# Optimization experiments

Hardware: AMD Instinct MI355X
Metric: run time of the kernel (lower is better)

Reference implementation:

```python
import jax, jax.numpy as jnp
import numpy as np

U = 100000          # unique pillars
N = 2 * U           # voxels (2 per pillar -> unq_cnt==2, mask all True)
NUM_BINS = 32       # z bins
C_IN = 5
C_HID = 32          # out_channels // 2 in conv1d MLP
C_OUT = 64
R = 4               # channel-attention reduction
K = 7               # bin-attention conv kernel


def setup_inputs() -> dict:
    key = jax.random.key(0)
    ks = jax.random.split(key, 12)
    voxel_features = jax.random.normal(ks[0], (N, C_IN), jnp.float32)
    # each pillar p owns voxels 2p, 2p+1 placed in two distinct bins -> no scatter collision
    bins = (jnp.arange(N, dtype=jnp.int32) % NUM_BINS)
    voxel_coords = jnp.zeros((N, 4), jnp.int32).at[:, 1].set(bins)
    unq_coords = jnp.arange(U, dtype=jnp.int32)
    unq_inv = jnp.arange(N, dtype=jnp.int32) // 2
    unq_cnt = jnp.full((U,), 2, jnp.int32)
    s = 0.3
    return {
        'voxel_features': voxel_features,
        'voxel_coords': voxel_coords,
        'unq_coords': unq_coords,
        'unq_inv': unq_inv,
        'unq_cnt': unq_cnt,
        # up_dimension MLP (Linear(5,32) -> relu -> Linear(32,64))
        'W1': jax.random.normal(ks[1], (C_IN, C_HID), jnp.float32) * s,
        'b1': jnp.zeros((C_HID,), jnp.float32),
        'W2': jax.random.normal(ks[2], (C_HID, C_OUT), jnp.float32) * s,
        'b2': jnp.zeros((C_OUT,), jnp.float32),
        # ZBAM channel-attention shared MLP
        'Wc1': jax.random.normal(ks[3], (C_OUT, C_OUT // R), jnp.float32) * s,
        'bc1': jnp.zeros((C_OUT // R,), jnp.float32),
        'Wc2': jax.random.normal(ks[4], (C_OUT // R, C_OUT), jnp.float32) * s,
        'bc2': jnp.zeros((C_OUT,), jnp.float32),
        # ZBAM bin (spatial) attention: conv1d over bins, 2->1 channels, kernel 7
        'Wsp': jax.random.normal(ks[5], (1, 2, K), jnp.float32) * s,
        'bsp': jnp.zeros((1,), jnp.float32),
    }


def _cbam_forward(voxel_features, W1, b1, W2, b2, Wc1, bc1, Wc2, bc2, Wsp, bsp,
                  voxel_coords, unq_coords, unq_inv, unq_cnt):
    n_pillars = unq_coords.shape[0]
    # --- binning: scatter voxels into (pillar, z-bin) slots ---
    src = jnp.zeros((n_pillars, NUM_BINS, voxel_features.shape[1]), voxel_features.dtype)
    src = src.at[unq_inv, voxel_coords[:, 1]].set(voxel_features)
    occupied_mask = unq_cnt >= 2  # all True by construction -> src[mask] == src
    # --- up_dimension MLP: (U, bins, 5) -> (U, bins, 64) ---
    x = jax.nn.relu(src @ W1 + b1) @ W2 + b2
    x = jnp.transpose(x, (0, 2, 1))  # (U, C, bins)
    # --- ZBAM channel attention ---
    avg_p = x.mean(axis=2)
    max_p = x.max(axis=2)
    mlp = lambda v: jax.nn.relu(v @ Wc1 + bc1) @ Wc2 + bc2
    att_c = jax.nn.sigmoid(mlp(avg_p) + mlp(max_p))  # (U, C)
    x = x * att_c[:, :, None]
    # --- ZBAM bin attention (conv over z-bins) ---
    s = jnp.stack([x.mean(axis=1), x.max(axis=1)], axis=1)  # (U, 2, bins)
    att_s = jax.lax.conv_general_dilated(
        s, Wsp, window_strides=(1,), padding=[(K // 2, K // 2)],
        dimension_numbers=('NCH', 'OIH', 'NCH')) + bsp  # (U, 1, bins)
    x = x * jax.nn.sigmoid(att_s)
    # --- max-pool over bins ---
    return x.max(axis=2), occupied_mask


def reference(voxel_features, voxel_coords, unq_coords, unq_inv, unq_cnt,
              W1, b1, W2, b2, Wc1, bc1, Wc2, bc2, Wsp, bsp):
    return _cbam_forward(voxel_features, W1, b1, W2, b2, Wc1, bc1, Wc2, bc2,
                         Wsp, bsp, voxel_coords, unq_coords, unq_inv, unq_cnt)
```

## Files before the change

kernel.cpp:

```cpp
#include <hip/hip_runtime.h>
#include <math.h>


#define CO 64

typedef __attribute__((ext_vector_type(8))) short s16x8;
typedef __attribute__((ext_vector_type(4))) float f32x4;
union ABu { uint4 u4; s16x8 s; };

__device__ __forceinline__ float sgm(float x) {
  return 1.0f / (1.0f + __expf(-x));
}
template <int PAT>
__device__ __forceinline__ float qadd(float s) {
  int t = __builtin_amdgcn_update_dpp(0, __builtin_bit_cast(int, s),
                                      PAT, 0xf, 0xf, true);
  return s + __builtin_bit_cast(float, t);
}
template <int PAT>
__device__ __forceinline__ float qmaxd(float m) {
  int t = __builtin_amdgcn_update_dpp(__builtin_bit_cast(int, m),
                                      __builtin_bit_cast(int, m),
                                      PAT, 0xf, 0xf, false);
  return fmaxf(m, __builtin_bit_cast(float, t));
}
template <int PAT>
__device__ __forceinline__ float qmind(float m) {
  int t = __builtin_amdgcn_update_dpp(__builtin_bit_cast(int, m),
                                      __builtin_bit_cast(int, m),
                                      PAT, 0xf, 0xf, false);
  return fminf(m, __builtin_bit_cast(float, t));
}
__device__ __forceinline__ float qsum4(float s) { return qadd<0x4E>(qadd<0xB1>(s)); }
__device__ __forceinline__ float qmax4(float m) { return qmaxd<0x4E>(qmaxd<0xB1>(m)); }
__device__ __forceinline__ float qmin4(float m) { return qmind<0x4E>(qmind<0xB1>(m)); }
__device__ __forceinline__ void drain_lds() {
  __builtin_amdgcn_wave_barrier();
  __builtin_amdgcn_s_waitcnt(0xC07F);
  __builtin_amdgcn_wave_barrier();
}
__device__ __forceinline__ void drain_vm() {
  __builtin_amdgcn_wave_barrier();
  __builtin_amdgcn_s_waitcnt(0x0F70);
  __builtin_amdgcn_wave_barrier();
}

__device__ __forceinline__ uint rtn16(float f) {
  uint u = __builtin_bit_cast(uint, f);
  return u + 0x7fffu + ((u >> 16) & 1u);
}
__device__ __forceinline__ void mk_frag(const float* e, ABu& hi, ABu& lo) {
  uint h[4], l[4];
#pragma unroll
  for (int p = 0; p < 4; ++p) {
    uint r0 = rtn16(e[2 * p]), r1 = rtn16(e[2 * p + 1]);
    h[p] = (r0 >> 16) | (r1 & 0xffff0000u);
    float d0 = e[2 * p]     - __builtin_bit_cast(float, r0 & 0xffff0000u);
    float d1 = e[2 * p + 1] - __builtin_bit_cast(float, r1 & 0xffff0000u);
    uint s0 = rtn16(d0), s1 = rtn16(d1);
    l[p] = (s0 >> 16) | (s1 & 0xffff0000u);
  }
  hi.u4 = make_uint4(h[0], h[1], h[2], h[3]);
  lo.u4 = make_uint4(l[0], l[1], l[2], l[3]);
}

__global__ __launch_bounds__(256) void pack_kernel(
    const float* __restrict__ vf, const int* __restrict__ vcoord,
    const int* __restrict__ unq_inv, float* __restrict__ pvox, int n) {
  int i = blockIdx.x * blockDim.x + threadIdx.x;
  if (i >= n) return;
  int p = unq_inv[i];
  int slot = (i > 0 && unq_inv[i - 1] == p) ? 1 : 0;
  float* dst = pvox + 8 * (size_t)(2 * p + slot);
#pragma unroll
  for (int k = 0; k < 5; ++k) dst[k] = vf[5 * i + k];
  ((int*)dst)[5] = vcoord[4 * i + 1];
}

__global__ __launch_bounds__(256) void cbam_kernel(
    const float* __restrict__ pvox, const int* __restrict__ unq_cnt,
    const float* __restrict__ W1, const float* __restrict__ b1,
    const float* __restrict__ W2, const float* __restrict__ b2,
    const float* __restrict__ Wc1, const float* __restrict__ bc1,
    const float* __restrict__ Wc2, const float* __restrict__ bc2,
    const float* __restrict__ Wsp, const float* __restrict__ bsp,
    float* __restrict__ out, int U, int ngroups, int totalWaves) {
  __shared__ __align__(16) uint4 w2fh[256], w2fl[256];
  __shared__ __align__(16) float w1b[160], b1b[32];
  __shared__ __align__(16) float wc1b[1024];
  __shared__ __align__(16) float wc2b[1024];
  __shared__ __align__(16) float c0b[64], b2b[64], bc2b[64], bc1b[16];
  __shared__ __align__(16) float wsmx[64];
  __shared__ __align__(16) float wtab[16];
  __shared__ __align__(16) float vbuf[4][256];
  __shared__ __align__(16) float2 ybuf[4][544];

  const int tid = threadIdx.x;

  {
    const int nt = tid >> 6, l = tid & 63, gg = l >> 4, cc = l & 15;
    uint hu[4], lu[4];
#pragma unroll
    for (int p = 0; p < 4; ++p) {
      float f0 = W2[(8 * gg + 2 * p)     * 64 + 16 * nt + cc];
      float f1 = W2[(8 * gg + 2 * p + 1) * 64 + 16 * nt + cc];
      uint r0 = rtn16(f0), r1 = rtn16(f1);
      hu[p] = (r0 >> 16) | (r1 & 0xffff0000u);
      float d0 = f0 - __builtin_bit_cast(float, r0 & 0xffff0000u);
      float d1 = f1 - __builtin_bit_cast(float, r1 & 0xffff0000u);
      uint s0 = rtn16(d0), s1 = rtn16(d1);
      lu[p] = (s0 >> 16) | (s1 & 0xffff0000u);
    }
    w2fh[tid] = make_uint4(hu[0], hu[1], hu[2], hu[3]);
    w2fl[tid] = make_uint4(lu[0], lu[1], lu[2], lu[3]);
  }
  if (tid < 160) w1b[tid] = W1[tid];
  if (tid < 32) b1b[tid] = b1[tid];
  for (int i = tid; i < 1024; i += 256) {
    int ch = i >> 4, j = i & 15, qq = ch >> 4, k = ch & 15;
    wc1b[(4 * k + qq) * 16 + j] = Wc1[i];
    wc2b[(4 * k + qq) * 16 + j] = Wc2[j * 64 + ch];
  }
  if (tid < 64) { b2b[tid] = b2[tid]; bc2b[tid] = bc2[tid]; }
  if (tid < 16) bc1b[tid] = bc1[tid];
  if (tid < 32) {
    float sm = 0.0f, sx = 0.0f;
    for (int k = 0; k < 7; ++k)
      if ((unsigned)(tid + k - 3) < 32u) { sm += Wsp[k]; sx += Wsp[7 + k]; }
    wsmx[2 * tid] = sm; wsmx[2 * tid + 1] = sx;
  }
  if (tid < 8) {
    float a = 0.0f, b = 0.0f;
    if (tid < 7) { a = Wsp[tid]; b = Wsp[7 + tid]; }
    wtab[2 * tid] = a; wtab[2 * tid + 1] = b;
  }
  __syncthreads();
  if (tid < 64) {
    float c = b2b[tid];
    for (int j = 0; j < 32; ++j) c += fmaxf(b1b[j], 0.0f) * W2[j * 64 + tid];
    c0b[tid] = c;
  }
  __syncthreads();

  const int wv = tid >> 6, lane = tid & 63;
  int grp = blockIdx.x * 4 + wv;
  if (grp >= ngroups) return;

  float* const vb = vbuf[wv];
  float4* const vb4 = (float4*)vb;
  float2* const yb2 = ybuf[wv];
  float4* const yb4 = (float4*)yb2;

  const int c16 = lane & 15, g = lane >> 4;
  const int q = lane & 3, pp = lane >> 2;
  const float4* pv4 = (const float4*)pvox;
  const int f4max = 4 * U - 1;

  {
    int idx = 64 * grp + lane;
    idx = idx < f4max ? idx : f4max;
    __builtin_amdgcn_global_load_lds(
        (const __attribute__((address_space(1))) void*)(pv4 + idx),
        (__attribute__((address_space(3))) void*)vb4, 16, 0, 0);
  }
  drain_vm();

  for (; grp < ngroups; grp += totalWaves) {
    int ofs0 = 0;
    asm volatile("" : "+s"(ofs0));

    const int P0 = grp * 16;

    const int pg = P0 + pp;
    const int pc = pg < U ? pg : (U - 1);
    const int cnt = unq_cnt[pc];
    const int* vbi = (const int*)vb;
    const int b0 = vbi[(2 * pp) * 8 + 5] & 31;
    const int b1raw = vbi[(2 * pp + 1) * 8 + 5];

    ABu ah0, al0, ah1, al1;
    {
      const float4* vb4c = (const float4*)vb;
      float4 xa = vb4c[2 * c16], xb = vb4c[2 * c16 + 1];
      float4 yc = vb4c[2 * (c16 + 16)], yd = vb4c[2 * (c16 + 16) + 1];
      float va[5] = {xa.x, xa.y, xa.z, xa.w, xb.x};
      float vc[5] = {yc.x, yc.y, yc.z, yc.w, yd.x};
      const float4* w1b4 = (const float4*)w1b;
      const float4* b1b4 = (const float4*)b1b;
      float4 bA = b1b4[ofs0 + 2 * g], bB = b1b4[ofs0 + 2 * g + 1];
      float e0[8] = {bA.x, bA.y, bA.z, bA.w, bB.x, bB.y, bB.z, bB.w};
      float e1[8] = {bA.x, bA.y, bA.z, bA.w, bB.x, bB.y, bB.z, bB.w};
#pragma unroll
      for (int d = 0; d < 5; ++d) {
        float4 w0 = w1b4[ofs0 + d * 8 + 2 * g];
        float4 w1v = w1b4[ofs0 + d * 8 + 2 * g + 1];
        e0[0] += va[d] * w0.x;  e0[1] += va[d] * w0.y;
        e0[2] += va[d] * w0.z;  e0[3] += va[d] * w0.w;
        e0[4] += va[d] * w1v.x; e0[5] += va[d] * w1v.y;
        e0[6] += va[d] * w1v.z; e0[7] += va[d] * w1v.w;
        e1[0] += vc[d] * w0.x;  e1[1] += vc[d] * w0.y;
        e1[2] += vc[d] * w0.z;  e1[3] += vc[d] * w0.w;
        e1[4] += vc[d] * w1v.x; e1[5] += vc[d] * w1v.y;
        e1[6] += vc[d] * w1v.z; e1[7] += vc[d] * w1v.w;
      }
#pragma unroll
      for (int i = 0; i < 8; ++i) {
        e0[i] = fmaxf(e0[i], 0.0f);
        e1[i] = fmaxf(e1[i], 0.0f);
      }
      mk_frag(e0, ah0, al0);
      mk_frag(e1, ah1, al1);
    }
    drain_lds();

    {
      const int nxt = grp + totalWaves;
      if (nxt < ngroups) {
        int nidx = 64 * nxt + lane;
        nidx = nidx < f4max ? nidx : f4max;
        __builtin_amdgcn_global_load_lds(
            (const __attribute__((address_space(1))) void*)(pv4 + nidx),
            (__attribute__((address_space(3))) void*)vb4, 16, 0, 0);
      }
    }

    float y0[16], y1[16];
#pragma unroll
    for (int half = 0; half < 2; ++half) {
      f32x4 acc[2][2];
#pragma unroll
      for (int mt = 0; mt < 2; ++mt)
#pragma unroll
        for (int ntp = 0; ntp < 2; ++ntp) acc[mt][ntp] = 0;
#pragma unroll
      for (int ntp = 0; ntp < 2; ++ntp) {
        const int nt = 2 * half + ntp;
        ABu bh, bl;
        bh.u4 = w2fh[ofs0 + nt * 64 + lane];
        bl.u4 = w2fl[ofs0 + nt * 64 + lane];
        acc[0][ntp] = __builtin_amdgcn_mfma_f32_16x16x32_bf16(ah0.s, bh.s, acc[0][ntp], 0, 0, 0);
        acc[0][ntp] = __builtin_amdgcn_mfma_f32_16x16x32_bf16(al0.s, bh.s, acc[0][ntp], 0, 0, 0);
        acc[0][ntp] = __builtin_amdgcn_mfma_f32_16x16x32_bf16(ah0.s, bl.s, acc[0][ntp], 0, 0, 0);
        acc[0][ntp] = __builtin_amdgcn_mfma_f32_16x16x32_bf16(al0.s, bl.s, acc[0][ntp], 0, 0, 0);
        acc[1][ntp] = __builtin_amdgcn_mfma_f32_16x16x32_bf16(ah1.s, bh.s, acc[1][ntp], 0, 0, 0);
        acc[1][ntp] = __builtin_amdgcn_mfma_f32_16x16x32_bf16(al1.s, bh.s, acc[1][ntp], 0, 0, 0);
        acc[1][ntp] = __builtin_amdgcn_mfma_f32_16x16x32_bf16(ah1.s, bl.s, acc[1][ntp], 0, 0, 0);
        acc[1][ntp] = __builtin_amdgcn_mfma_f32_16x16x32_bf16(al1.s, bl.s, acc[1][ntp], 0, 0, 0);
      }
#pragma unroll
      for (int ntp = 0; ntp < 2; ++ntp) {
        const float b2v = b2b[16 * (2 * half + ntp) + c16];
#pragma unroll
        for (int mt = 0; mt < 2; ++mt)
#pragma unroll
          for (int rp = 0; rp < 2; ++rp) {
            const int p = 8 * mt + 2 * g + rp;
            float2 v2;
            v2.x = acc[mt][ntp][2 * rp]     + b2v;
            v2.y = acc[mt][ntp][2 * rp + 1] + b2v;
            yb2[p * 34 + 16 * ntp + c16] = v2;
          }
      }
      if ((q >> 1) == half) {
#pragma unroll
        for (int kk = 0; kk < 8; ++kk) {
          float4 t = yb4[pp * 17 + 8 * (q & 1) + kk];
          y0[2 * kk]     = t.x; y1[2 * kk]     = t.y;
          y0[2 * kk + 1] = t.z; y1[2 * kk + 1] = t.w;
        }
      }
      drain_lds();
    }

    const bool has2 = (cnt >= 2);
    const int b1e = has2 ? (b1raw & 31) : 64;
#pragma unroll
    for (int k = 0; k < 16; ++k) y1[k] = has2 ? y1[k] : y0[k];

    float ha[16] = {0}, hm[16] = {0};
    const float kf = has2 ? 30.0f : 31.0f;
    const float inv32 = 1.0f / 32.0f;
    const float4* c04 = (const float4*)c0b;
    const float4* wc14 = (const float4*)wc1b;
#pragma unroll
    for (int kb = 0; kb < 4; ++kb) {
      float4 cq = c04[q * 4 + kb];
      float c0a[4] = {cq.x, cq.y, cq.z, cq.w};
#pragma unroll
      for (int i = 0; i < 4; ++i) {
        const int k = 4 * kb + i;
        const float c0v = c0a[i];
        const float sumy = y0[k] + (has2 ? y1[k] : 0.0f);
        const float avg = fmaf(c0v, kf, sumy) * inv32;
        const float mxv = fmaxf(fmaxf(y0[k], y1[k]), c0v);
#pragma unroll
        for (int jb = 0; jb < 4; ++jb) {
          float4 w = wc14[(4 * k + q) * 4 + jb];
          ha[4 * jb]     += avg * w.x; ha[4 * jb + 1] += avg * w.y;
          ha[4 * jb + 2] += avg * w.z; ha[4 * jb + 3] += avg * w.w;
          hm[4 * jb]     += mxv * w.x; hm[4 * jb + 1] += mxv * w.y;
          hm[4 * jb + 2] += mxv * w.z; hm[4 * jb + 3] += mxv * w.w;
        }
      }
    }
    float gq[16];
    const float4* bc14 = (const float4*)bc1b;
#pragma unroll
    for (int jb = 0; jb < 4; ++jb) {
      float4 bb = bc14[jb];
      float bba[4] = {bb.x, bb.y, bb.z, bb.w};
#pragma unroll
      for (int i = 0; i < 4; ++i) {
        const int j = 4 * jb + i;
        const float sa = qsum4(ha[j]) + bba[i];
        const float sm = qsum4(hm[j]) + bba[i];
        gq[j] = fmaxf(sa, 0.0f) + fmaxf(sm, 0.0f);
      }
    }

    float attc[16];
    float sc = 0.0f, mc = -3.0e38f;
    float sy0 = 0.0f, my0 = -3.0e38f, sy1 = 0.0f, my1 = -3.0e38f;
    const float4* wc24 = (const float4*)wc2b;
    const float4* bc24 = (const float4*)bc2b;
#pragma unroll
    for (int kb = 0; kb < 4; ++kb) {
      float4 cq = c04[q * 4 + kb];
      float4 bq = bc24[q * 4 + kb];
      float c0a[4] = {cq.x, cq.y, cq.z, cq.w};
      float b2a[4] = {bq.x, bq.y, bq.z, bq.w};
#pragma unroll
      for (int i = 0; i < 4; ++i) {
        const int k = 4 * kb + i;
        float pre = 2.0f * b2a[i];
#pragma unroll
        for (int jb = 0; jb < 4; ++jb) {
          float4 w = wc24[(4 * k + q) * 4 + jb];
          pre += gq[4 * jb] * w.x + gq[4 * jb + 1] * w.y +
                 gq[4 * jb + 2] * w.z + gq[4 * jb + 3] * w.w;
        }
        const float a = sgm(pre);
        attc[k] = a;
        const float pc0 = a * c0a[i], py0 = a * y0[k], py1 = a * y1[k];
        sc += pc0;  mc = fmaxf(mc, pc0);
        sy0 += py0; my0 = fmaxf(my0, py0);
        sy1 += py1; my1 = fmaxf(my1, py1);
      }
    }
    sc = qsum4(sc);   mc = qmax4(mc);
    sy0 = qsum4(sy0); my0 = qmax4(my0);
    sy1 = qsum4(sy1); my1 = qmax4(my1);

    const float inv64 = 1.0f / 64.0f;
    const float Mn = sc * inv64, Mx = mc;
    const float dm0 = (sy0 - sc) * inv64, dx0 = my0 - mc;
    const float dm1 = (sy1 - sc) * inv64, dx1 = my1 - mc;
    const float bspr = bsp[0];
    const float2* ws2 = (const float2*)wsmx;
    const float2* wt2 = (const float2*)wtab;
    float maxE = -3.0e38f, minE = 3.0e38f, sv0 = -3.0e38f, sv1 = -3.0e38f;
#pragma unroll
    for (int k = 0; k < 8; ++k) {
      const int b = 8 * q + k;
      float2 ws = ws2[b];
      float acc2 = bspr + Mn * ws.x + Mx * ws.y;
      int k0 = b0 - b + 3;  k0 = ((unsigned)k0 <= 6u) ? k0 : 7;
      int k1 = b1e - b + 3; k1 = ((unsigned)k1 <= 6u) ? k1 : 7;
      float2 w0 = wt2[k0];
      float2 w1v = wt2[k1];
      acc2 += dm0 * w0.x + dx0 * w0.y + dm1 * w1v.x + dx1 * w1v.y;
      const bool o0 = (b == b0), o1 = (b == b1e);
      const bool oc = o0 || o1;
      maxE = fmaxf(maxE, oc ? -3.0e38f : acc2);
      minE = fminf(minE, oc ?  3.0e38f : acc2);
      sv0 = o0 ? acc2 : sv0;
      sv1 = o1 ? acc2 : sv1;
    }
    maxE = qmax4(maxE); minE = qmin4(minE);
    sv0 = qmax4(sv0);   sv1 = qmax4(sv1);
    const float sig0 = sgm(sv0);
    const float sig1 = has2 ? sgm(sv1) : sig0;
    const float sE = sgm(maxE), sI = sgm(minE);

    if (pg < U) {
      float4* ov = (float4*)(out + (size_t)pg * CO + 16 * q);
#pragma unroll
      for (int kb = 0; kb < 4; ++kb) {
        float4 cq = c04[q * 4 + kb];
        float c0a[4] = {cq.x, cq.y, cq.z, cq.w};
        float rr[4];
#pragma unroll
        for (int i = 0; i < 4; ++i) {
          const int k = 4 * kb + i;
          const float c0v = c0a[i];
          const float sel = (c0v >= 0.0f) ? sE : sI;
          const float m = fmaxf(fmaxf(y0[k] * sig0, y1[k] * sig1), c0v * sel);
          rr[i] = attc[k] * m;
        }
        float4 r; r.x = rr[0]; r.y = rr[1]; r.z = rr[2]; r.w = rr[3];
        ov[kb] = r;
      }
      if (q == 0) out[(size_t)U * CO + pg] = has2 ? 1.0f : 0.0f;
    }

    drain_vm();
  }
}

extern "C" void kernel_launch(void* const* d_in, const int* in_sizes, int n_in,
                              void* d_out, int out_size, void* d_ws, size_t ws_size,
                              hipStream_t stream) {
  const float* vf      = (const float*)d_in[0];
  const int*   vcoord  = (const int*)d_in[1];
  const int*   unq_inv = (const int*)d_in[3];
  const int*   unq_cnt = (const int*)d_in[4];
  const float* W1  = (const float*)d_in[5];
  const float* b1  = (const float*)d_in[6];
  const float* W2  = (const float*)d_in[7];
  const float* b2  = (const float*)d_in[8];
  const float* Wc1 = (const float*)d_in[9];
  const float* bc1 = (const float*)d_in[10];
  const float* Wc2 = (const float*)d_in[11];
  const float* bc2 = (const float*)d_in[12];
  const float* Wsp = (const float*)d_in[13];
  const float* bsp = (const float*)d_in[14];

  const int N = in_sizes[3];
  const int U = in_sizes[4];

  float* pvox = (float*)d_ws;

  pack_kernel<<<(N + 255) / 256, 256, 0, stream>>>(vf, vcoord, unq_inv, pvox, N);

  static int blocksPerCU = 0;
  if (blocksPerCU == 0) {
    hipFuncAttributes a{};
    blocksPerCU = 4;
    if (hipFuncGetAttributes(&a, (const void*)cbam_kernel) == hipSuccess) {
      int byV = (a.numRegs > 0) ? (512 / a.numRegs) : 4;
      int byL = (a.sharedSizeBytes > 0)
                    ? (int)(163840 / (int)a.sharedSizeBytes) : 4;
      int m = byV < byL ? byV : byL;
      if (m < 1) m = 1;
      if (m > 8) m = 8;
      blocksPerCU = m;
    }
  }

  const int ngroups = (U + 15) / 16;
  int blocks = 256 * blocksPerCU;
  const int maxBlocks = (ngroups + 3) / 4;
  if (blocks > maxBlocks) blocks = maxBlocks;
  const int totalWaves = blocks * 4;
  cbam_kernel<<<blocks, 256, 0, stream>>>(
      pvox, unq_cnt, W1, b1, W2, b2, Wc1, bc1, Wc2, bc2, Wsp, bsp,
      (float*)d_out, U, ngroups, totalWaves);
}
```

Before: 137.7 us.

## Cut register pressure: per-tile MFMA epilogue, split channel-MLP accumulators, hardware bf16 pack

Replaces the software round-to-nearest bf16 split with the v_cvt_pk_bf16_f32 instruction. Restructures the W2 MFMA stage to handle one 16-column tile at a time with a smaller LDS staging buffer, and drops the per-half LDS drain. Splits the channel-attention hidden accumulators into two passes of 8, so fewer registers are live. Rounds the register count to allocation granularity when sizing the grid. The goal is fewer VGPRs and higher occupancy. The cost is removing the LDS drain between tile write and read, which relies on compiler-inserted waits for correctness, plus a second pass over the y values.

Result: no change. 138.7 us (+0.8%).

```diff
diff --git a/kernel.cpp b/kernel.cpp
--- a/kernel.cpp
+++ b/kernel.cpp
@@ -49,16 +49,19 @@
   uint u = __builtin_bit_cast(uint, f);
   return u + 0x7fffu + ((u >> 16) & 1u);
 }
+__device__ __forceinline__ uint cvtpk(float a, float b) {
+  uint r;
+  asm("v_cvt_pk_bf16_f32 %0, %1, %2" : "=v"(r) : "v"(a), "v"(b));
+  return r;
+}
 __device__ __forceinline__ void mk_frag(const float* e, ABu& hi, ABu& lo) {
   uint h[4], l[4];
 #pragma unroll
   for (int p = 0; p < 4; ++p) {
-    uint r0 = rtn16(e[2 * p]), r1 = rtn16(e[2 * p + 1]);
-    h[p] = (r0 >> 16) | (r1 & 0xffff0000u);
-    float d0 = e[2 * p]     - __builtin_bit_cast(float, r0 & 0xffff0000u);
-    float d1 = e[2 * p + 1] - __builtin_bit_cast(float, r1 & 0xffff0000u);
-    uint s0 = rtn16(d0), s1 = rtn16(d1);
-    l[p] = (s0 >> 16) | (s1 & 0xffff0000u);
+    h[p] = cvtpk(e[2 * p], e[2 * p + 1]);
+    float d0 = e[2 * p]     - __builtin_bit_cast(float, h[p] << 16);
+    float d1 = e[2 * p + 1] - __builtin_bit_cast(float, h[p] & 0xffff0000u);
+    l[p] = cvtpk(d0, d1);
   }
   hi.u4 = make_uint4(h[0], h[1], h[2], h[3]);
   lo.u4 = make_uint4(l[0], l[1], l[2], l[3]);
@@ -93,7 +96,7 @@
   __shared__ __align__(16) float wsmx[64];
   __shared__ __align__(16) float wtab[16];
   __shared__ __align__(16) float vbuf[4][256];
-  __shared__ __align__(16) float2 ybuf[4][544];
+  __shared__ __align__(16) float4 ybuf[4][144];
 
   const int tid = threadIdx.x;
 
@@ -148,8 +151,8 @@
 
   float* const vb = vbuf[wv];
   float4* const vb4 = (float4*)vb;
-  float2* const yb2 = ybuf[wv];
-  float4* const yb4 = (float4*)yb2;
+  float4* const yb4 = ybuf[wv];
+  float2* const yb2 = (float2*)yb4;
 
   const int c16 = lane & 15, g = lane >> 4;
   const int q = lane & 3, pp = lane >> 2;
@@ -226,50 +229,39 @@
 
     float y0[16], y1[16];
 #pragma unroll
-    for (int half = 0; half < 2; ++half) {
-      f32x4 acc[2][2];
+    for (int nt = 0; nt < 4; ++nt) {
+      ABu bh, bl;
+      bh.u4 = w2fh[ofs0 + nt * 64 + lane];
+      bl.u4 = w2fl[ofs0 + nt * 64 + lane];
+      f32x4 acc[2];
+      acc[0] = 0; acc[1] = 0;
+      acc[0] = __builtin_amdgcn_mfma_f32_16x16x32_bf16(ah0.s, bh.s, acc[0], 0, 0, 0);
+      acc[0] = __builtin_amdgcn_mfma_f32_16x16x32_bf16(al0.s, bh.s, acc[0], 0, 0, 0);
+      acc[0] = __builtin_amdgcn_mfma_f32_16x16x32_bf16(ah0.s, bl.s, acc[0], 0, 0, 0);
+      acc[0] = __builtin_amdgcn_mfma_f32_16x16x32_bf16(al0.s, bl.s, acc[0], 0, 0, 0);
+      acc[1] = __builtin_amdgcn_mfma_f32_16x16x32_bf16(ah1.s, bh.s, acc[1], 0, 0, 0);
+      acc[1] = __builtin_amdgcn_mfma_f32_16x16x32_bf16(al1.s, bh.s, acc[1], 0, 0, 0);
+      acc[1] = __builtin_amdgcn_mfma_f32_16x16x32_bf16(ah1.s, bl.s, acc[1], 0, 0, 0);
+      acc[1] = __builtin_amdgcn_mfma_f32_16x16x32_bf16(al1.s, bl.s, acc[1], 0, 0, 0);
+      const float b2v = b2b[16 * nt + c16];
 #pragma unroll
       for (int mt = 0; mt < 2; ++mt)
 #pragma unroll
-        for (int ntp = 0; ntp < 2; ++ntp) acc[mt][ntp] = 0;
-#pragma unroll
-      for (int ntp = 0; ntp < 2; ++ntp) {
-        const int nt = 2 * half + ntp;
-        ABu bh, bl;
-        bh.u4 = w2fh[ofs0 + nt * 64 + lane];
-        bl.u4 = w2fl[ofs0 + nt * 64 + lane];
-        acc[0][ntp] = __builtin_amdgcn_mfma_f32_16x16x32_bf16(ah0.s, bh.s, acc[0][ntp], 0, 0, 0);
-        acc[0][ntp] = __builtin_amdgcn_mfma_f32_16x16x32_bf16(al0.s, bh.s, acc[0][ntp], 0, 0, 0);
-        acc[0][ntp] = __builtin_amdgcn_mfma_f32_16x16x32_bf16(ah0.s, bl.s, acc[0][ntp], 0, 0, 0);
-        acc[0][ntp] = __builtin_amdgcn_mfma_f32_16x16x32_bf16(al0.s, bl.s, acc[0][ntp], 0, 0, 0);
-        acc[1][ntp] = __builtin_amdgcn_mfma_f32_16x16x32_bf16(ah1.s, bh.s, acc[1][ntp], 0, 0, 0);
-        acc[1][ntp] = __builtin_amdgcn_mfma_f32_16x16x32_bf16(al1.s, bh.s, acc[1][ntp], 0, 0, 0);
-        acc[1][ntp] = __builtin_amdgcn_mfma_f32_16x16x32_bf16(ah1.s, bl.s, acc[1][ntp], 0, 0, 0);
-        acc[1][ntp] = __builtin_amdgcn_mfma_f32_16x16x32_bf16(al1.s, bl.s, acc[1][ntp], 0, 0, 0);
-      }
-#pragma unroll
-      for (int ntp = 0; ntp < 2; ++ntp) {
-        const float b2v = b2b[16 * (2 * half + ntp) + c16];
-#pragma unroll
-        for (int mt = 0; mt < 2; ++mt)
-#pragma unroll
-          for (int rp = 0; rp < 2; ++rp) {
-            const int p = 8 * mt + 2 * g + rp;
-            float2 v2;
-            v2.x = acc[mt][ntp][2 * rp]     + b2v;
-            v2.y = acc[mt][ntp][2 * rp + 1] + b2v;
-            yb2[p * 34 + 16 * ntp + c16] = v2;
-          }
-      }
-      if ((q >> 1) == half) {
+        for (int rp = 0; rp < 2; ++rp) {
+          const int p = 8 * mt + 2 * g + rp;
+          float2 v2;
+          v2.x = acc[mt][2 * rp]     + b2v;
+          v2.y = acc[mt][2 * rp + 1] + b2v;
+          yb2[p * 18 + c16] = v2;
+        }
+      if (q == nt) {
 #pragma unroll
         for (int kk = 0; kk < 8; ++kk) {
-          float4 t = yb4[pp * 17 + 8 * (q & 1) + kk];
+          float4 t = yb4[pp * 9 + kk];
           y0[2 * kk]     = t.x; y1[2 * kk]     = t.y;
           y0[2 * kk + 1] = t.z; y1[2 * kk + 1] = t.w;
         }
       }
-      drain_lds();
     }
 
     const bool has2 = (cnt >= 2);
@@ -277,44 +269,46 @@
 #pragma unroll
     for (int k = 0; k < 16; ++k) y1[k] = has2 ? y1[k] : y0[k];
 
-    float ha[16] = {0}, hm[16] = {0};
+    float gq[16];
     const float kf = has2 ? 30.0f : 31.0f;
     const float inv32 = 1.0f / 32.0f;
     const float4* c04 = (const float4*)c0b;
     const float4* wc14 = (const float4*)wc1b;
-#pragma unroll
-    for (int kb = 0; kb < 4; ++kb) {
-      float4 cq = c04[q * 4 + kb];
-      float c0a[4] = {cq.x, cq.y, cq.z, cq.w};
-#pragma unroll
-      for (int i = 0; i < 4; ++i) {
-        const int k = 4 * kb + i;
-        const float c0v = c0a[i];
-        const float sumy = y0[k] + (has2 ? y1[k] : 0.0f);
-        const float avg = fmaf(c0v, kf, sumy) * inv32;
-        const float mxv = fmaxf(fmaxf(y0[k], y1[k]), c0v);
-#pragma unroll
-        for (int jb = 0; jb < 4; ++jb) {
-          float4 w = wc14[(4 * k + q) * 4 + jb];
-          ha[4 * jb]     += avg * w.x; ha[4 * jb + 1] += avg * w.y;
-          ha[4 * jb + 2] += avg * w.z; ha[4 * jb + 3] += avg * w.w;
-          hm[4 * jb]     += mxv * w.x; hm[4 * jb + 1] += mxv * w.y;
-          hm[4 * jb + 2] += mxv * w.z; hm[4 * jb + 3] += mxv * w.w;
-        }
-      }
-    }
-    float gq[16];
     const float4* bc14 = (const float4*)bc1b;
 #pragma unroll
-    for (int jb = 0; jb < 4; ++jb) {
-      float4 bb = bc14[jb];
-      float bba[4] = {bb.x, bb.y, bb.z, bb.w};
-#pragma unroll
-      for (int i = 0; i < 4; ++i) {
-        const int j = 4 * jb + i;
-        const float sa = qsum4(ha[j]) + bba[i];
-        const float sm = qsum4(hm[j]) + bba[i];
-        gq[j] = fmaxf(sa, 0.0f) + fmaxf(sm, 0.0f);
+    for (int jp = 0; jp < 2; ++jp) {
+      float ha[8] = {0}, hm[8] = {0};
+#pragma unroll
+      for (int kb = 0; kb < 4; ++kb) {
+        float4 cq = c04[q * 4 + kb];
+        float c0a[4] = {cq.x, cq.y, cq.z, cq.w};
+#pragma unroll
+        for (int i = 0; i < 4; ++i) {
+          const int k = 4 * kb + i;
+          const float c0v = c0a[i];
+          const float sumy = y0[k] + (has2 ? y1[k] : 0.0f);
+          const float avg = fmaf(c0v, kf, sumy) * inv32;
+          const float mxv = fmaxf(fmaxf(y0[k], y1[k]), c0v);
+#pragma unroll
+          for (int jbl = 0; jbl < 2; ++jbl) {
+            float4 w = wc14[(4 * k + q) * 4 + 2 * jp + jbl];
+            ha[4 * jbl]     += avg * w.x; ha[4 * jbl + 1] += avg * w.y;
+            ha[4 * jbl + 2] += avg * w.z; ha[4 * jbl + 3] += avg * w.w;
+            hm[4 * jbl]     += mxv * w.x; hm[4 * jbl + 1] += mxv * w.y;
+            hm[4 * jbl + 2] += mxv * w.z; hm[4 * jbl + 3] += mxv * w.w;
+          }
+        }
+      }
+#pragma unroll
+      for (int jbl = 0; jbl < 2; ++jbl) {
+        float4 bb = bc14[2 * jp + jbl];
+        float bba[4] = {bb.x, bb.y, bb.z, bb.w};
+#pragma unroll
+        for (int i = 0; i < 4; ++i) {
+          const float sa = qsum4(ha[4 * jbl + i]) + bba[i];
+          const float sm = qsum4(hm[4 * jbl + i]) + bba[i];
+          gq[8 * jp + 4 * jbl + i] = fmaxf(sa, 0.0f) + fmaxf(sm, 0.0f);
+        }
       }
     }
 
@@ -437,7 +431,8 @@
     hipFuncAttributes a{};
     blocksPerCU = 4;
     if (hipFuncGetAttributes(&a, (const void*)cbam_kernel) == hipSuccess) {
-      int byV = (a.numRegs > 0) ? (512 / a.numRegs) : 4;
+      int v8 = (a.numRegs > 0) ? ((a.numRegs + 7) & ~7) : 128;
+      int byV = 512 / v8;
       int byL = (a.sharedSizeBytes > 0)
                     ? (int)(163840 / (int)a.sharedSizeBytes) : 4;
       int m = byV < byL ? byV : byL;
```
